# Optimization experiments

Hardware: AMD Instinct MI355X
Metric: run time of the kernel (lower is better)

The kernel has to match this reference:

```python
import jax, jax.numpy as jnp
import numpy as np

B = 8192          # batch_size = len(embedds)
D = 512           # ll_p['num_channels'][-1]
C = 100           # n_classes
N_LAB = 4096      # int(B * plb), plb = 0.5
MAX_ITER = 30     # gtg_i
TOL = 1e-3        # gtg_t
ENT_EPS = 1e-20


def _mlp(x, W1, b1, W2, b2, W3, b3, Wc, bc):
    h = jax.nn.relu(x @ W1 + b1)
    h = jax.nn.relu(h @ W2 + b2)
    h = jax.nn.relu(h @ W3 + b3)
    return (h @ Wc + bc)[:, 0]  # squeeze -> [B]


def _entropy(X):
    # per-row Shannon entropy (bits), as in ALGTG utils
    return -jnp.sum(X * jnp.log2(X + ENT_EPS), axis=1)


def _gtg_entropy_hist(embedds, labels):
    # get_A: cos_sim -> zero diagonal -> clamp [0,1] -> 'mean' threshold -> 'diversity' (1-A)
    n = jnp.maximum(jnp.linalg.norm(embedds, axis=-1, keepdims=True), 1e-12)
    E = embedds / n
    A = E @ E.T                                   # [B,B]
    A = A * (1.0 - jnp.eye(B, dtype=A.dtype))     # fill_diagonal_(0)
    A = jnp.clip(A, 0.0, 1.0)
    A = jnp.where(A < jnp.mean(A), 0.0, A)        # AM_threshold_strategy == 'mean'
    A = 1.0 - A                                   # AM_strategy == 'diversity'

    # get_X: labeled rows one-hot, unlabeled rows uniform 1/C
    lab = jnp.arange(B) < N_LAB
    X0 = jnp.where(lab[:, None],
                   jax.nn.one_hot(labels, C, dtype=jnp.float32),
                   jnp.full((B, C), 1.0 / C, jnp.float32))
    hist0 = jnp.zeros((B, MAX_ITER), jnp.float32)
    unlab = ~lab

    def cond(s):
        _X, _h, i, err = s
        return (err > TOL) & (i < MAX_ITER)

    def body(s):
        X, hist, i, _err = s
        Xn = X * (A @ X)                          # replicator dynamics step
        Xn = Xn / jnp.sum(Xn, axis=1, keepdims=True)
        ent = _entropy(Xn)
        hist = hist.at[:, i].set(jnp.where(unlab, ent, 0.0))
        return (Xn, hist, i + 1, jnp.linalg.norm(Xn - X))

    init = (X0, hist0, jnp.array(0, jnp.int32), jnp.array(jnp.inf, jnp.float32))
    _, hist, _, _ = jax.lax.while_loop(cond, body, init)
    return hist


def setup_inputs() -> dict:
    key = jax.random.key(0)
    ks = jax.random.split(key, 11)
    d2, d4, d8 = D // 2, D // 4, D // 8

    def lin(k, fi, fo):
        return jax.random.normal(k, (fi, fo), jnp.float32) / np.float32(np.sqrt(fi))

    return {
        'features': jax.random.normal(ks[0], (B, 64), jnp.float32),
        'embedds': jax.random.normal(ks[1], (B, D), jnp.float32),
        'labels': jax.random.randint(ks[2], (B,), 0, C),
        'W1': lin(ks[3], D, d2), 'b1': jnp.zeros((d2,), jnp.float32),
        'W2': lin(ks[4], d2, d4), 'b2': jnp.zeros((d4,), jnp.float32),
        'W3': lin(ks[5], d4, d8), 'b3': jnp.zeros((d8,), jnp.float32),
        'Wc': lin(ks[6], d8, 1), 'bc': jnp.zeros((1,), jnp.float32),
    }


def reference(features, embedds, labels, W1, b1, W2, b2, W3, b3, Wc, bc):
    y_pred = _mlp(embedds, W1, b1, W2, b2, W3, b3, Wc, bc)        # [B]
    hist = _gtg_entropy_hist(embedds, labels)                      # [B, MAX_ITER]
    y_true = jnp.mean(hist, axis=1)                                # ent_strategy == 'mean'
    labeled_mask = jnp.arange(B) < N_LAB                           # bool [B]
    return (y_pred, y_true, labeled_mask)
```

## Files before the change

### kernel.cpp

```cpp
#include <hip/hip_runtime.h>
#include <hip/hip_bf16.h>
#include <math.h>

namespace {
constexpr int BROWS = 8192;
constexpr int NLAB  = 4096;
constexpr int NUNL  = 4096;
constexpr int CREAL = 100;
constexpr int CPAD  = 112;
constexpr int DIM   = 512;
constexpr int MAXIT = 30;

constexpr size_t MiB = 1ull << 20;
constexpr size_t OFF_S    = 0;
constexpr size_t OFF_AU   = 64 * MiB;
constexpr size_t OFF_EB   = 96 * MiB;
constexpr size_t OFF_XT0  = 96 * MiB;
constexpr size_t OFF_XT1  = 98 * MiB;
constexpr size_t OFF_XU   = 100 * MiB;
constexpr size_t OFF_PL   = 102 * MiB;
constexpr size_t OFF_HIST = 104 * MiB;
constexpr size_t OFF_ERR  = 104 * MiB + 16384;
constexpr size_t OFF_MS   = 104 * MiB + 16768;
constexpr size_t OFF_RN   = 104 * MiB + 32768;
constexpr size_t MEMSET_LEN = 20480;
}

typedef __attribute__((ext_vector_type(8))) short short8;
typedef __attribute__((ext_vector_type(4))) float floatx4;

__device__ inline ushort f2bf(float f) {
  __hip_bfloat16 h = __float2bfloat16(f);
  union { __hip_bfloat16 b; ushort u; } c; c.b = h; return c.u;
}
__device__ inline float bf2f(ushort u) {
  union { ushort u; __hip_bfloat16 b; } c; c.u = u;
  return __bfloat162float(c.b);
}

__global__ __launch_bounds__(64) void k_prep(const float* __restrict__ emb,
                                             ushort* __restrict__ Eb,
                                             float* __restrict__ rn) {
  int row = blockIdx.x, l = threadIdx.x;
  const float4* e4 = (const float4*)(emb + (size_t)row * DIM);
  float4 a = e4[2 * l], b = e4[2 * l + 1];
  float f[8] = {a.x, a.y, a.z, a.w, b.x, b.y, b.z, b.w};
  float s = 0.f;
#pragma unroll
  for (int q = 0; q < 8; q++) s += f[q] * f[q];
#pragma unroll
  for (int m = 1; m < 64; m <<= 1) s += __shfl_xor(s, m);
  if (l == 0) rn[row] = 1.0f / fmaxf(sqrtf(s), 1e-12f);
  union { short8 v; ushort u[8]; } o;
#pragma unroll
  for (int q = 0; q < 8; q++) o.u[q] = f2bf(f[q]);
  *(short8*)(Eb + (size_t)row * DIM + l * 8) = o.v;
}

__global__ __launch_bounds__(256) void k_initX(ushort* __restrict__ X0,
                                               ushort* __restrict__ X1,
                                               float* __restrict__ Xu,
                                               const int* __restrict__ labels) {
  int j = blockIdx.x * 256 + threadIdx.x;
  int c = blockIdx.y;
  float v;
  if (j < NLAB) v = (labels[j] == c) ? 1.0f : 0.0f;
  else          v = (c < CREAL) ? 0.01f : 0.0f;
  ushort b = f2bf(v);
  X0[(size_t)c * BROWS + j] = b;
  X1[(size_t)c * BROWS + j] = b;
  if (j >= NLAB) Xu[(size_t)(j - NLAB) * CPAD + c] = (c < CREAL) ? 0.01f : 0.0f;
}

__global__ __launch_bounds__(256) void k_mlp(const float* __restrict__ emb,
                                             const float* __restrict__ W1, const float* __restrict__ b1,
                                             const float* __restrict__ W2, const float* __restrict__ b2,
                                             const float* __restrict__ W3, const float* __restrict__ b3,
                                             const float* __restrict__ Wc, const float* __restrict__ bc,
                                             float* __restrict__ out) {
  __shared__ float xs[16][512];
  __shared__ float h1[16][256];
  __shared__ float h2[16][128];
  __shared__ float h3[16][64];
  int t = threadIdx.x;
  int r0 = blockIdx.x * 16;
  {
    const float4* src = (const float4*)(emb + (size_t)r0 * DIM);
    float4* dst = (float4*)&xs[0][0];
#pragma unroll
    for (int q = 0; q < 8; q++) dst[t + q * 256] = src[t + q * 256];
  }
  __syncthreads();
  {
    float a[16];
#pragma unroll
    for (int r = 0; r < 16; r++) a[r] = 0.f;
    for (int k = 0; k < 512; k++) {
      float wv = W1[k * 256 + t];
#pragma unroll
      for (int r = 0; r < 16; r++) a[r] = fmaf(xs[r][k], wv, a[r]);
    }
    float bb = b1[t];
#pragma unroll
    for (int r = 0; r < 16; r++) h1[r][t] = fmaxf(a[r] + bb, 0.f);
  }
  __syncthreads();
  {
    int c = t & 127, rb = (t >> 7) * 8;
    float a[8];
#pragma unroll
    for (int r = 0; r < 8; r++) a[r] = 0.f;
    for (int k = 0; k < 256; k++) {
      float wv = W2[k * 128 + c];
#pragma unroll
      for (int r = 0; r < 8; r++) a[r] = fmaf(h1[rb + r][k], wv, a[r]);
    }
    float bb = b2[c];
#pragma unroll
    for (int r = 0; r < 8; r++) h2[rb + r][c] = fmaxf(a[r] + bb, 0.f);
  }
  __syncthreads();
  {
    int c = t & 63, rb = (t >> 6) * 4;
    float a[4];
#pragma unroll
    for (int r = 0; r < 4; r++) a[r] = 0.f;
    for (int k = 0; k < 128; k++) {
      float wv = W3[k * 64 + c];
#pragma unroll
      for (int r = 0; r < 4; r++) a[r] = fmaf(h2[rb + r][k], wv, a[r]);
    }
#pragma unroll
    for (int r = 0; r < 4; r++) h3[rb + r][c] = fmaxf(a[r] + b3[c], 0.f);
  }
  __syncthreads();
  {
    int w = t >> 6, l = t & 63;
#pragma unroll
    for (int rr = 0; rr < 4; rr++) {
      int r = w * 4 + rr;
      float v = h3[r][l] * Wc[l];
#pragma unroll
      for (int mm = 32; mm; mm >>= 1) v += __shfl_down(v, mm);
      if (l == 0) out[r0 + r] = v + bc[0];
    }
  }
}

__global__ __launch_bounds__(256) void k_simM(const ushort* __restrict__ Eb,
                                              const float* __restrict__ rn,
                                              ushort* __restrict__ S,
                                              double* __restrict__ meansum) {
  int x = blockIdx.x, y = blockIdx.y;
  if (x < 32 && y > x) return;
  __shared__ ushort Ei[128 * 40];
  __shared__ ushort Ej[128 * 40];
  __shared__ float redbuf[4];

  int t = threadIdx.x;
  int w = t >> 6, lane = t & 63;
  int m = lane & 15, g = lane >> 4;
  int ib = (w >> 1) * 64, jb = (w & 1) * 64;
  int i0 = x * 128, j0 = y * 128;

  floatx4 acc[4][4];
#pragma unroll
  for (int a = 0; a < 4; a++)
#pragma unroll
    for (int b = 0; b < 4; b++) acc[a][b] = (floatx4)0.0f;

  int lrow = t >> 1, lhalf = (t & 1) * 16;
  for (int kt = 0; kt < DIM; kt += 32) {
    __syncthreads();
    {
      const ushort* gi = Eb + (size_t)(i0 + lrow) * DIM + kt + lhalf;
      const ushort* gj = Eb + (size_t)(j0 + lrow) * DIM + kt + lhalf;
      int o = lrow * 40 + lhalf;
      *(short8*)&Ei[o]     = *(const short8*)gi;
      *(short8*)&Ei[o + 8] = *(const short8*)(gi + 8);
      *(short8*)&Ej[o]     = *(const short8*)gj;
      *(short8*)&Ej[o + 8] = *(const short8*)(gj + 8);
    }
    __syncthreads();

    short8 ah[4], bh[4];
#pragma unroll
    for (int rt = 0; rt < 4; rt++) ah[rt] = *(const short8*)&Ei[(ib + rt * 16 + m) * 40 + g * 8];
#pragma unroll
    for (int ct = 0; ct < 4; ct++) bh[ct] = *(const short8*)&Ej[(jb + ct * 16 + m) * 40 + g * 8];
#pragma unroll
    for (int rt = 0; rt < 4; rt++)
#pragma unroll
      for (int ct = 0; ct < 4; ct++)
        acc[rt][ct] = __builtin_amdgcn_mfma_f32_16x16x32_bf16(ah[rt], bh[ct], acc[rt][ct], 0, 0, 0);
  }

  bool dostore = (x >= 32);
  bool isdiag  = (x == y);
  float weight = (x < 32) ? (isdiag ? 1.0f : 2.0f) : ((y < 32) ? 2.0f : 1.0f);
  float lsum = 0.f;
#pragma unroll
  for (int rt = 0; rt < 4; rt++) {
    int gi0 = i0 + ib + rt * 16 + g * 4;
    float4 rni = *(const float4*)(rn + gi0);
#pragma unroll
    for (int ct = 0; ct < 4; ct++) {
      int gj = j0 + jb + ct * 16 + m;
      float rnj = rn[gj];
#pragma unroll
      for (int r = 0; r < 4; r++) {
        int gi = gi0 + r;
        float rv = (r == 0) ? rni.x : (r == 1) ? rni.y : (r == 2) ? rni.z : rni.w;
        float s = acc[rt][ct][r] * rv * rnj;
        if (isdiag && gi == gj) s = 0.f;
        s = fminf(fmaxf(s, 0.f), 1.f);
        lsum += s;
        if (dostore) S[(size_t)(gi - NLAB) * BROWS + gj] = f2bf(s);
      }
    }
  }
  lsum *= weight;
#pragma unroll
  for (int d = 1; d < 64; d <<= 1) lsum += __shfl_xor(lsum, d);
  if (lane == 0) redbuf[w] = lsum;
  __syncthreads();
  if (t == 0) atomicAdd(meansum, (double)(redbuf[0] + redbuf[1] + redbuf[2] + redbuf[3]));
}

__global__ __launch_bounds__(1024, 4) void k_iter(const ushort* __restrict__ S,
                                                  ushort* __restrict__ Au,
                                                  const ushort* __restrict__ XTr,
                                                  ushort* __restrict__ XTw,
                                                  float* __restrict__ Xu,
                                                  float* __restrict__ Plab,
                                                  float* __restrict__ hist,
                                                  float* __restrict__ errsq,
                                                  const double* __restrict__ ms,
                                                  int it) {
  if (it > 0 && errsq[it - 1] <= 1e-6f) return;
  __shared__ float part[4][32 * 113];
  __shared__ float dsqb[16];
  float*  Pbuf = &part[0][0];
  ushort* xbuf = (ushort*)((char*)&part[0][0] + 16384);

  int t = threadIdx.x;
  int w = t >> 6, lane = t & 63;
  int m = lane & 15, g = lane >> 4;
  int r0 = blockIdx.x * 32;

  float2 xo[2];
  xo[0] = make_float2(0.f, 0.f); xo[1] = make_float2(0.f, 0.f);
  if (lane < 56) {
    xo[0] = *(const float2*)(Xu + (size_t)(r0 + w * 2)     * CPAD + lane * 2);
    xo[1] = *(const float2*)(Xu + (size_t)(r0 + w * 2 + 1) * CPAD + lane * 2);
  }
  float pl_pre[4] = {0.f, 0.f, 0.f, 0.f};
  if (it > 0) {
#pragma unroll
    for (int q = 0; q < 4; q++) {
      int idx = t + q * 1024;
      if (idx < 32 * CPAD)
        pl_pre[q] = Plab[(size_t)(r0 + idx / CPAD) * CPAD + idx % CPAD];
    }
  }

  floatx4 acc[2][7];
#pragma unroll
  for (int rt = 0; rt < 2; rt++)
#pragma unroll
    for (int c = 0; c < 7; c++) acc[rt][c] = (floatx4)0.0f;

  if (it == 0) {
    float mean = (float)(ms[0] * (1.0 / ((double)BROWS * (double)BROWS)));
    int kw = w * 512;
    for (int ks = 0; ks < 16; ks++) {
      int kk = kw + ks * 32;
      short8 a[2];
#pragma unroll
      for (int rt = 0; rt < 2; rt++) {
        size_t so = (size_t)(r0 + rt * 16 + m) * BROWS + kk + g * 8;
        union { short8 v; ushort u[8]; } ua;
        ua.v = *(const short8*)(S + so);
#pragma unroll
        for (int e = 0; e < 8; e++) {
          float s = bf2f(ua.u[e]);
          float av = (s < mean) ? 1.0f : 1.0f - s;
          ua.u[e] = f2bf(av);
        }
        a[rt] = ua.v;
        if (w >= 8)
          *(short8*)(Au + (size_t)(r0 + rt * 16 + m) * NUNL + (kk - NLAB) + g * 8) = a[rt];
      }
#pragma unroll
      for (int ct = 0; ct < 7; ct++) {
        short8 b = *(const short8*)(XTr + (size_t)(ct * 16 + m) * BROWS + kk + g * 8);
        acc[0][ct] = __builtin_amdgcn_mfma_f32_16x16x32_bf16(a[0], b, acc[0][ct], 0, 0, 0);
        acc[1][ct] = __builtin_amdgcn_mfma_f32_16x16x32_bf16(a[1], b, acc[1][ct], 0, 0, 0);
      }
    }
  } else {
    int kw = w * 256;
    size_t a0b = (size_t)(r0 + m)      * NUNL + kw + g * 8;
    size_t a1b = (size_t)(r0 + 16 + m) * NUNL + kw + g * 8;
    size_t bb  = (size_t)m * BROWS + NLAB + kw + g * 8;
    for (int ks = 0; ks < 8; ks++) {
      short8 a0 = *(const short8*)(Au + a0b + ks * 32);
      short8 a1 = *(const short8*)(Au + a1b + ks * 32);
#pragma unroll
      for (int ct = 0; ct < 7; ct++) {
        short8 b = *(const short8*)(XTr + bb + (size_t)ct * 16 * BROWS + ks * 32);
        acc[0][ct] = __builtin_amdgcn_mfma_f32_16x16x32_bf16(a0, b, acc[0][ct], 0, 0, 0);
        acc[1][ct] = __builtin_amdgcn_mfma_f32_16x16x32_bf16(a1, b, acc[1][ct], 0, 0, 0);
      }
    }
  }

  float sA[4], sB[4];
  for (int p = 0; p < 4; p++) {
    if ((w >> 2) == p) {
#pragma unroll
      for (int rt = 0; rt < 2; rt++)
#pragma unroll
        for (int ct = 0; ct < 7; ct++)
#pragma unroll
          for (int r = 0; r < 4; r++)
            part[w & 3][(rt * 16 + g * 4 + r) * 113 + ct * 16 + m] = acc[rt][ct][r];
    }
    __syncthreads();
#pragma unroll
    for (int q = 0; q < 4; q++) {
      int idx = t + q * 1024;
      if (idx < 32 * CPAD) {
        int o = (idx / CPAD) * 113 + idx % CPAD;
        float s = (part[0][o] + part[1][o]) + (part[2][o] + part[3][o]);
        if (p == 0) sA[q] = s;
        else if (p == 1) sA[q] += s;
        else if (p == 2) sB[q] = s;
        else sB[q] += s;
      }
    }
    __syncthreads();
  }

#pragma unroll
  for (int q = 0; q < 4; q++) {
    int idx = t + q * 1024;
    if (idx < 32 * CPAD) {
      int row = idx / CPAD, col = idx % CPAD;
      float P;
      if (it == 0) { Plab[(size_t)(r0 + row) * CPAD + col] = sA[q]; P = sA[q] + sB[q]; }
      else         { P = sA[q] + sB[q] + pl_pre[q]; }
      Pbuf[row * 114 + col] = P;
    }
  }
  __syncthreads();

  bool act = lane < 56;
  float dtot = 0.f;
#pragma unroll
  for (int rr = 0; rr < 2; rr++) {
    int rw = w * 2 + rr;
    int gr = r0 + rw;
    float2 p = make_float2(0.f, 0.f);
    if (act) p = *(const float2*)&Pbuf[rw * 114 + lane * 2];
    float2 xn;
    xn.x = xo[rr].x * p.x;
    xn.y = xo[rr].y * p.y;
    float s = xn.x + xn.y;
#pragma unroll
    for (int d = 1; d < 64; d <<= 1) s += __shfl_xor(s, d);
    float inv = 1.0f / s;
    float ent = 0.f, dsq = 0.f;
    if (act) {
      xn.x *= inv; xn.y *= inv;
      ent = -(xn.x * log2f(xn.x + 1e-20f) + xn.y * log2f(xn.y + 1e-20f));
      float dx = xn.x - xo[rr].x, dy = xn.y - xo[rr].y;
      dsq = dx * dx + dy * dy;
      *(float2*)(Xu + (size_t)gr * CPAD + lane * 2) = xn;
      int c0 = lane * 2;
      xbuf[c0 * 34 + rw]       = f2bf(xn.x);
      xbuf[(c0 + 1) * 34 + rw] = f2bf(xn.y);
    }
#pragma unroll
    for (int d = 1; d < 64; d <<= 1) { ent += __shfl_xor(ent, d); dsq += __shfl_xor(dsq, d); }
    if (lane == 0) hist[gr] += ent;
    dtot += dsq;
  }
  if (lane == 0) dsqb[w] = dtot;
  __syncthreads();

#pragma unroll
  for (int q = 0; q < 2; q++) {
    int tt = t + q * 1024;
    if (tt < CPAD * 16) {
      int c = tt >> 4, jl = (tt & 15) * 2;
      ushort2 v = *(const ushort2*)&xbuf[c * 34 + jl];
      *(ushort2*)(XTw + (size_t)c * BROWS + NLAB + r0 + jl) = v;
    }
  }
  if (t == 0) {
    float ds = 0.f;
#pragma unroll
    for (int i = 0; i < 16; i++) ds += dsqb[i];
    atomicAdd(&errsq[it], ds);
  }
}

__global__ __launch_bounds__(256) void k_final(const float* __restrict__ hist,
                                               float* __restrict__ out) {
  int i = blockIdx.x * 256 + threadIdx.x;
  float yt = (i < NLAB) ? 0.0f : hist[i - NLAB] * (1.0f / 30.0f);
  out[BROWS + i] = yt;
  out[2 * BROWS + i] = (i < NLAB) ? 1.0f : 0.0f;
}

extern "C" void kernel_launch(void* const* d_in, const int* in_sizes, int n_in,
                              void* d_out, int out_size, void* d_ws, size_t ws_size,
                              hipStream_t stream) {
  const float* emb    = (const float*)d_in[1];
  const int*   labels = (const int*)d_in[2];
  const float* W1 = (const float*)d_in[3];
  const float* b1 = (const float*)d_in[4];
  const float* W2 = (const float*)d_in[5];
  const float* b2 = (const float*)d_in[6];
  const float* W3 = (const float*)d_in[7];
  const float* b3 = (const float*)d_in[8];
  const float* Wc = (const float*)d_in[9];
  const float* bc = (const float*)d_in[10];
  float* out = (float*)d_out;

  char* ws = (char*)d_ws;
  ushort* S    = (ushort*)(ws + OFF_S);
  ushort* Au   = (ushort*)(ws + OFF_AU);
  ushort* Eb   = (ushort*)(ws + OFF_EB);
  ushort* XT0  = (ushort*)(ws + OFF_XT0);
  ushort* XT1  = (ushort*)(ws + OFF_XT1);
  float*  Xu   = (float*)(ws + OFF_XU);
  float*  Plab = (float*)(ws + OFF_PL);
  float*  hist = (float*)(ws + OFF_HIST);
  float*  errs = (float*)(ws + OFF_ERR);
  double* ms   = (double*)(ws + OFF_MS);
  float*  rn   = (float*)(ws + OFF_RN);

  hipMemsetAsync(ws + OFF_HIST, 0, MEMSET_LEN, stream);

  k_prep<<<BROWS, 64, 0, stream>>>(emb, Eb, rn);
  k_mlp<<<BROWS / 16, 256, 0, stream>>>(emb, W1, b1, W2, b2, W3, b3, Wc, bc, out);

  { dim3 g(BROWS / 128, BROWS / 128); k_simM<<<g, 256, 0, stream>>>(Eb, rn, S, ms); }

  { dim3 g(BROWS / 256, CPAD); k_initX<<<g, 256, 0, stream>>>(XT0, XT1, Xu, labels); }

  for (int it = 0; it < MAXIT; it++) {
    const ushort* XTr = (it & 1) ? XT1 : XT0;
    ushort*       XTw = (it & 1) ? XT0 : XT1;
    k_iter<<<NUNL / 32, 1024, 0, stream>>>(S, Au, XTr, XTw, Xu, Plab, hist, errs, ms, it);
  }

  k_final<<<BROWS / 256, 256, 0, stream>>>(hist, out);
}
```

Baseline: 799.5 us.

## Halve row tile per block in iteration and MLP kernels, add nontemporal A loads

The iteration kernel now handles 16 unlabeled rows per block instead of 32, which doubles the grid to 256 blocks and restructures the partial-sum reduction into two 8-way LDS passes. The MLP kernel handles 4 rows per block instead of 16, giving four times as many blocks. Loads of the similarity and A matrices use nontemporal hints to avoid polluting cache. The aim is better occupancy and CU coverage on the memory-bound iteration, at the cost of reading the X^T operand twice as often across blocks.

```diff
diff --git a/kernel.cpp b/kernel.cpp
--- a/kernel.cpp
+++ b/kernel.cpp
@@ -37,6 +37,9 @@
   union { ushort u; __hip_bfloat16 b; } c; c.u = u;
   return __bfloat162float(c.b);
 }
+__device__ inline short8 ntload_s8(const ushort* p) {
+  return __builtin_nontemporal_load((const short8*)p);
+}
 
 __global__ __launch_bounds__(64) void k_prep(const float* __restrict__ emb,
                                              ushort* __restrict__ Eb,
@@ -78,72 +81,61 @@
                                              const float* __restrict__ W3, const float* __restrict__ b3,
                                              const float* __restrict__ Wc, const float* __restrict__ bc,
                                              float* __restrict__ out) {
-  __shared__ float xs[16][512];
-  __shared__ float h1[16][256];
-  __shared__ float h2[16][128];
-  __shared__ float h3[16][64];
+  __shared__ float xs[4][512];
+  __shared__ float h1[4][256];
+  __shared__ float h2[4][128];
+  __shared__ float h3[4][64];
   int t = threadIdx.x;
-  int r0 = blockIdx.x * 16;
+  int r0 = blockIdx.x * 4;
   {
     const float4* src = (const float4*)(emb + (size_t)r0 * DIM);
     float4* dst = (float4*)&xs[0][0];
-#pragma unroll
-    for (int q = 0; q < 8; q++) dst[t + q * 256] = src[t + q * 256];
+    dst[t] = src[t];
+    dst[t + 256] = src[t + 256];
   }
   __syncthreads();
   {
-    float a[16];
-#pragma unroll
-    for (int r = 0; r < 16; r++) a[r] = 0.f;
+    float a0 = 0.f, a1 = 0.f, a2 = 0.f, a3 = 0.f;
     for (int k = 0; k < 512; k++) {
-      float wv = W1[k * 256 + t];
-#pragma unroll
-      for (int r = 0; r < 16; r++) a[r] = fmaf(xs[r][k], wv, a[r]);
+      float w = W1[k * 256 + t];
+      a0 = fmaf(xs[0][k], w, a0);
+      a1 = fmaf(xs[1][k], w, a1);
+      a2 = fmaf(xs[2][k], w, a2);
+      a3 = fmaf(xs[3][k], w, a3);
     }
     float bb = b1[t];
-#pragma unroll
-    for (int r = 0; r < 16; r++) h1[r][t] = fmaxf(a[r] + bb, 0.f);
+    h1[0][t] = fmaxf(a0 + bb, 0.f);
+    h1[1][t] = fmaxf(a1 + bb, 0.f);
+    h1[2][t] = fmaxf(a2 + bb, 0.f);
+    h1[3][t] = fmaxf(a3 + bb, 0.f);
   }
   __syncthreads();
   {
-    int c = t & 127, rb = (t >> 7) * 8;
-    float a[8];
-#pragma unroll
-    for (int r = 0; r < 8; r++) a[r] = 0.f;
+    int c = t & 127, rb = (t >> 7) * 2;
+    float a0 = 0.f, a1 = 0.f;
     for (int k = 0; k < 256; k++) {
-      float wv = W2[k * 128 + c];
-#pragma unroll
-      for (int r = 0; r < 8; r++) a[r] = fmaf(h1[rb + r][k], wv, a[r]);
+      float w = W2[k * 128 + c];
+      a0 = fmaf(h1[rb][k], w, a0);
+      a1 = fmaf(h1[rb + 1][k], w, a1);
     }
     float bb = b2[c];
-#pragma unroll
-    for (int r = 0; r < 8; r++) h2[rb + r][c] = fmaxf(a[r] + bb, 0.f);
+    h2[rb][c] = fmaxf(a0 + bb, 0.f);
+    h2[rb + 1][c] = fmaxf(a1 + bb, 0.f);
   }
   __syncthreads();
   {
-    int c = t & 63, rb = (t >> 6) * 4;
-    float a[4];
-#pragma unroll
-    for (int r = 0; r < 4; r++) a[r] = 0.f;
-    for (int k = 0; k < 128; k++) {
-      float wv = W3[k * 64 + c];
-#pragma unroll
-      for (int r = 0; r < 4; r++) a[r] = fmaf(h2[rb + r][k], wv, a[r]);
-    }
-#pragma unroll
-    for (int r = 0; r < 4; r++) h3[rb + r][c] = fmaxf(a[r] + b3[c], 0.f);
+    int c = t & 63, r = t >> 6;
+    float a = 0.f;
+    for (int k = 0; k < 128; k++) a = fmaf(h2[r][k], W3[k * 64 + c], a);
+    h3[r][c] = fmaxf(a + b3[c], 0.f);
   }
   __syncthreads();
   {
-    int w = t >> 6, l = t & 63;
-#pragma unroll
-    for (int rr = 0; rr < 4; rr++) {
-      int r = w * 4 + rr;
-      float v = h3[r][l] * Wc[l];
-#pragma unroll
-      for (int mm = 32; mm; mm >>= 1) v += __shfl_down(v, mm);
-      if (l == 0) out[r0 + r] = v + bc[0];
-    }
+    int r = t >> 6, l = t & 63;
+    float v = h3[r][l] * Wc[l];
+#pragma unroll
+    for (int m = 32; m; m >>= 1) v += __shfl_down(v, m);
+    if (l == 0) out[r0 + r] = v + bc[0];
   }
 }
 
@@ -238,170 +230,152 @@
                                                   const double* __restrict__ ms,
                                                   int it) {
   if (it > 0 && errsq[it - 1] <= 1e-6f) return;
-  __shared__ float part[4][32 * 113];
-  __shared__ float dsqb[16];
-  float*  Pbuf = &part[0][0];
-  ushort* xbuf = (ushort*)((char*)&part[0][0] + 16384);
-
+  __shared__ float part[8][16 * 113];
+  __shared__ float Pbuf[16 * 114];
+  __shared__ float dsqbuf[16];
+  ushort* xbuf = (ushort*)&part[0][0];
   int t = threadIdx.x;
   int w = t >> 6, lane = t & 63;
   int m = lane & 15, g = lane >> 4;
-  int r0 = blockIdx.x * 32;
-
-  float2 xo[2];
-  xo[0] = make_float2(0.f, 0.f); xo[1] = make_float2(0.f, 0.f);
-  if (lane < 56) {
-    xo[0] = *(const float2*)(Xu + (size_t)(r0 + w * 2)     * CPAD + lane * 2);
-    xo[1] = *(const float2*)(Xu + (size_t)(r0 + w * 2 + 1) * CPAD + lane * 2);
-  }
-  float pl_pre[4] = {0.f, 0.f, 0.f, 0.f};
+  int r0 = blockIdx.x * 16;
+
+  float2 xo = make_float2(0.f, 0.f);
+  if (lane < 56) xo = *(const float2*)(Xu + (size_t)(r0 + w) * CPAD + lane * 2);
+  float pl_pre[2] = {0.f, 0.f};
   if (it > 0) {
 #pragma unroll
-    for (int q = 0; q < 4; q++) {
+    for (int q = 0; q < 2; q++) {
       int idx = t + q * 1024;
-      if (idx < 32 * CPAD)
+      if (idx < 16 * CPAD)
         pl_pre[q] = Plab[(size_t)(r0 + idx / CPAD) * CPAD + idx % CPAD];
     }
   }
 
-  floatx4 acc[2][7];
-#pragma unroll
-  for (int rt = 0; rt < 2; rt++)
-#pragma unroll
-    for (int c = 0; c < 7; c++) acc[rt][c] = (floatx4)0.0f;
+  floatx4 acc[7];
+#pragma unroll
+  for (int c = 0; c < 7; c++) acc[c] = (floatx4)0.0f;
 
   if (it == 0) {
     float mean = (float)(ms[0] * (1.0 / ((double)BROWS * (double)BROWS)));
     int kw = w * 512;
     for (int ks = 0; ks < 16; ks++) {
       int kk = kw + ks * 32;
-      short8 a[2];
-#pragma unroll
-      for (int rt = 0; rt < 2; rt++) {
-        size_t so = (size_t)(r0 + rt * 16 + m) * BROWS + kk + g * 8;
-        union { short8 v; ushort u[8]; } ua;
-        ua.v = *(const short8*)(S + so);
-#pragma unroll
-        for (int e = 0; e < 8; e++) {
-          float s = bf2f(ua.u[e]);
-          float av = (s < mean) ? 1.0f : 1.0f - s;
-          ua.u[e] = f2bf(av);
-        }
-        a[rt] = ua.v;
-        if (w >= 8)
-          *(short8*)(Au + (size_t)(r0 + rt * 16 + m) * NUNL + (kk - NLAB) + g * 8) = a[rt];
+      size_t so = (size_t)(r0 + m) * BROWS + kk + g * 8;
+      short8 a = ntload_s8(S + so);
+      union { short8 v; ushort u[8]; } ua; ua.v = a;
+#pragma unroll
+      for (int e = 0; e < 8; e++) {
+        float s = bf2f(ua.u[e]);
+        float av = (s < mean) ? 1.0f : 1.0f - s;
+        ua.u[e] = f2bf(av);
       }
+      a = ua.v;
+      if (w >= 8)
+        *(short8*)(Au + (size_t)(r0 + m) * NUNL + (kk - NLAB) + g * 8) = a;
 #pragma unroll
       for (int ct = 0; ct < 7; ct++) {
         short8 b = *(const short8*)(XTr + (size_t)(ct * 16 + m) * BROWS + kk + g * 8);
-        acc[0][ct] = __builtin_amdgcn_mfma_f32_16x16x32_bf16(a[0], b, acc[0][ct], 0, 0, 0);
-        acc[1][ct] = __builtin_amdgcn_mfma_f32_16x16x32_bf16(a[1], b, acc[1][ct], 0, 0, 0);
+        acc[ct] = __builtin_amdgcn_mfma_f32_16x16x32_bf16(a, b, acc[ct], 0, 0, 0);
       }
     }
   } else {
     int kw = w * 256;
-    size_t a0b = (size_t)(r0 + m)      * NUNL + kw + g * 8;
-    size_t a1b = (size_t)(r0 + 16 + m) * NUNL + kw + g * 8;
-    size_t bb  = (size_t)m * BROWS + NLAB + kw + g * 8;
+    size_t abase = (size_t)(r0 + m) * NUNL + kw + g * 8;
+    size_t bbase = (size_t)m * BROWS + NLAB + kw + g * 8;
     for (int ks = 0; ks < 8; ks++) {
-      short8 a0 = *(const short8*)(Au + a0b + ks * 32);
-      short8 a1 = *(const short8*)(Au + a1b + ks * 32);
+      short8 a = ntload_s8(Au + abase + ks * 32);
 #pragma unroll
       for (int ct = 0; ct < 7; ct++) {
-        short8 b = *(const short8*)(XTr + bb + (size_t)ct * 16 * BROWS + ks * 32);
-        acc[0][ct] = __builtin_amdgcn_mfma_f32_16x16x32_bf16(a0, b, acc[0][ct], 0, 0, 0);
-        acc[1][ct] = __builtin_amdgcn_mfma_f32_16x16x32_bf16(a1, b, acc[1][ct], 0, 0, 0);
+        short8 b = *(const short8*)(XTr + bbase + (size_t)ct * 16 * BROWS + ks * 32);
+        acc[ct] = __builtin_amdgcn_mfma_f32_16x16x32_bf16(a, b, acc[ct], 0, 0, 0);
       }
     }
   }
 
-  float sA[4], sB[4];
-  for (int p = 0; p < 4; p++) {
-    if ((w >> 2) == p) {
-#pragma unroll
-      for (int rt = 0; rt < 2; rt++)
-#pragma unroll
-        for (int ct = 0; ct < 7; ct++)
-#pragma unroll
-          for (int r = 0; r < 4; r++)
-            part[w & 3][(rt * 16 + g * 4 + r) * 113 + ct * 16 + m] = acc[rt][ct][r];
-    }
-    __syncthreads();
-#pragma unroll
-    for (int q = 0; q < 4; q++) {
-      int idx = t + q * 1024;
-      if (idx < 32 * CPAD) {
-        int o = (idx / CPAD) * 113 + idx % CPAD;
-        float s = (part[0][o] + part[1][o]) + (part[2][o] + part[3][o]);
-        if (p == 0) sA[q] = s;
-        else if (p == 1) sA[q] += s;
-        else if (p == 2) sB[q] = s;
-        else sB[q] += s;
-      }
-    }
-    __syncthreads();
-  }
-
-#pragma unroll
-  for (int q = 0; q < 4; q++) {
+  if (w < 8) {
+#pragma unroll
+    for (int ct = 0; ct < 7; ct++)
+#pragma unroll
+      for (int r = 0; r < 4; r++)
+        part[w][(g * 4 + r) * 113 + ct * 16 + m] = acc[ct][r];
+  }
+  __syncthreads();
+  float sA[2] = {0.f, 0.f}, sB[2] = {0.f, 0.f};
+#pragma unroll
+  for (int q = 0; q < 2; q++) {
     int idx = t + q * 1024;
-    if (idx < 32 * CPAD) {
+    if (idx < 16 * CPAD) {
       int row = idx / CPAD, col = idx % CPAD;
+      int o = row * 113 + col;
+      sA[q] = ((part[0][o] + part[1][o]) + (part[2][o] + part[3][o]))
+            + ((part[4][o] + part[5][o]) + (part[6][o] + part[7][o]));
+    }
+  }
+  __syncthreads();
+  if (w >= 8) {
+#pragma unroll
+    for (int ct = 0; ct < 7; ct++)
+#pragma unroll
+      for (int r = 0; r < 4; r++)
+        part[w - 8][(g * 4 + r) * 113 + ct * 16 + m] = acc[ct][r];
+  }
+  __syncthreads();
+#pragma unroll
+  for (int q = 0; q < 2; q++) {
+    int idx = t + q * 1024;
+    if (idx < 16 * CPAD) {
+      int row = idx / CPAD, col = idx % CPAD;
+      int o = row * 113 + col;
+      sB[q] = ((part[0][o] + part[1][o]) + (part[2][o] + part[3][o]))
+            + ((part[4][o] + part[5][o]) + (part[6][o] + part[7][o]));
       float P;
-      if (it == 0) { Plab[(size_t)(r0 + row) * CPAD + col] = sA[q]; P = sA[q] + sB[q]; }
+      size_t go = (size_t)(r0 + row) * CPAD + col;
+      if (it == 0) { Plab[go] = sA[q]; P = sA[q] + sB[q]; }
       else         { P = sA[q] + sB[q] + pl_pre[q]; }
       Pbuf[row * 114 + col] = P;
     }
   }
   __syncthreads();
 
+  int gr = r0 + w;
   bool act = lane < 56;
-  float dtot = 0.f;
-#pragma unroll
-  for (int rr = 0; rr < 2; rr++) {
-    int rw = w * 2 + rr;
-    int gr = r0 + rw;
-    float2 p = make_float2(0.f, 0.f);
-    if (act) p = *(const float2*)&Pbuf[rw * 114 + lane * 2];
-    float2 xn;
-    xn.x = xo[rr].x * p.x;
-    xn.y = xo[rr].y * p.y;
-    float s = xn.x + xn.y;
-#pragma unroll
-    for (int d = 1; d < 64; d <<= 1) s += __shfl_xor(s, d);
-    float inv = 1.0f / s;
-    float ent = 0.f, dsq = 0.f;
-    if (act) {
-      xn.x *= inv; xn.y *= inv;
-      ent = -(xn.x * log2f(xn.x + 1e-20f) + xn.y * log2f(xn.y + 1e-20f));
-      float dx = xn.x - xo[rr].x, dy = xn.y - xo[rr].y;
-      dsq = dx * dx + dy * dy;
-      *(float2*)(Xu + (size_t)gr * CPAD + lane * 2) = xn;
-      int c0 = lane * 2;
-      xbuf[c0 * 34 + rw]       = f2bf(xn.x);
-      xbuf[(c0 + 1) * 34 + rw] = f2bf(xn.y);
-    }
-#pragma unroll
-    for (int d = 1; d < 64; d <<= 1) { ent += __shfl_xor(ent, d); dsq += __shfl_xor(dsq, d); }
-    if (lane == 0) hist[gr] += ent;
-    dtot += dsq;
-  }
-  if (lane == 0) dsqb[w] = dtot;
-  __syncthreads();
-
-#pragma unroll
-  for (int q = 0; q < 2; q++) {
-    int tt = t + q * 1024;
-    if (tt < CPAD * 16) {
-      int c = tt >> 4, jl = (tt & 15) * 2;
-      ushort2 v = *(const ushort2*)&xbuf[c * 34 + jl];
-      *(ushort2*)(XTw + (size_t)c * BROWS + NLAB + r0 + jl) = v;
-    }
+  float2 p = make_float2(0.f, 0.f);
+  if (act) p = *(const float2*)&Pbuf[w * 114 + lane * 2];
+  float2 xn;
+  xn.x = xo.x * p.x;
+  xn.y = xo.y * p.y;
+  float s = xn.x + xn.y;
+#pragma unroll
+  for (int d = 1; d < 64; d <<= 1) s += __shfl_xor(s, d);
+  float inv = 1.0f / s;
+  float ent = 0.f, dsq = 0.f;
+  if (act) {
+    xn.x *= inv; xn.y *= inv;
+    ent = -(xn.x * log2f(xn.x + 1e-20f) + xn.y * log2f(xn.y + 1e-20f));
+    float dx = xn.x - xo.x, dy = xn.y - xo.y;
+    dsq = dx * dx + dy * dy;
+    *(float2*)(Xu + (size_t)gr * CPAD + lane * 2) = xn;
+    int c0 = lane * 2;
+    xbuf[c0 * 18 + w]       = f2bf(xn.x);
+    xbuf[(c0 + 1) * 18 + w] = f2bf(xn.y);
+  }
+#pragma unroll
+  for (int d = 1; d < 64; d <<= 1) { ent += __shfl_xor(ent, d); dsq += __shfl_xor(dsq, d); }
+  if (lane == 0) {
+    hist[gr] += ent;
+    dsqbuf[w] = dsq;
+  }
+  __syncthreads();
+
+  if (t < CPAD * 8) {
+    int c = t >> 3, jl = (t & 7) * 2;
+    ushort2 v = *(const ushort2*)&xbuf[c * 18 + jl];
+    *(ushort2*)(XTw + (size_t)c * BROWS + NLAB + r0 + jl) = v;
   }
   if (t == 0) {
     float ds = 0.f;
 #pragma unroll
-    for (int i = 0; i < 16; i++) ds += dsqb[i];
+    for (int i = 0; i < 16; i++) ds += dsqbuf[i];
     atomicAdd(&errsq[it], ds);
   }
 }
@@ -445,7 +419,7 @@
   hipMemsetAsync(ws + OFF_HIST, 0, MEMSET_LEN, stream);
 
   k_prep<<<BROWS, 64, 0, stream>>>(emb, Eb, rn);
-  k_mlp<<<BROWS / 16, 256, 0, stream>>>(emb, W1, b1, W2, b2, W3, b3, Wc, bc, out);
+  k_mlp<<<BROWS / 4, 256, 0, stream>>>(emb, W1, b1, W2, b2, W3, b3, Wc, bc, out);
 
   { dim3 g(BROWS / 128, BROWS / 128); k_simM<<<g, 256, 0, stream>>>(Eb, rn, S, ms); }
 
@@ -454,7 +428,7 @@
   for (int it = 0; it < MAXIT; it++) {
     const ushort* XTr = (it & 1) ? XT1 : XT0;
     ushort*       XTw = (it & 1) ? XT0 : XT1;
-    k_iter<<<NUNL / 32, 1024, 0, stream>>>(S, Au, XTr, XTw, Xu, Plab, hist, errs, ms, it);
+    k_iter<<<NUNL / 16, 1024, 0, stream>>>(S, Au, XTr, XTw, Xu, Plab, hist, errs, ms, it);
   }
 
   k_final<<<BROWS / 256, 256, 0, stream>>>(hist, out);
```

Measured after the change: 779.4 us. 1.03x faster.
